# Kernel tuning notes

Hardware: AMD Instinct MI355X
Metric: run time of the kernel (lower is better)

Reference implementation:

```python
import jax, jax.numpy as jnp
import numpy as np

D_MODEL = 1024
D_INTERNAL = 1024
B, T = 4, 2048
ROPE_BASE = 10000.0


def _rotate_half(x):
    h = x.shape[-1] // 2
    return jnp.concatenate([-x[..., h:], x[..., :h]], axis=-1)


def _justnorm(x):
    return x / jnp.linalg.norm(x, axis=-1, keepdims=True)


def setup_inputs() -> dict:
    key = jax.random.key(0)
    k1, k2 = jax.random.split(key)
    stdev = 1.0 / (D_MODEL + D_INTERNAL) ** 0.5
    qkv_w = jax.random.uniform(k1, (3 * D_INTERNAL, D_MODEL), minval=-stdev, maxval=stdev, dtype=jnp.float32)
    qkv_w = _justnorm(qkv_w)  # source normalizes qkv rows at init
    sqk = (D_MODEL ** -0.5) * jnp.ones((D_INTERNAL,), dtype=jnp.float32)  # sqk_init_scaling * ones
    input_vecs = jax.random.normal(k2, (B, T, D_MODEL), dtype=jnp.float32)
    return {"input_vecs": input_vecs, "qkv_w": qkv_w, "sqk": sqk}


def reference(input_vecs, qkv_w, sqk):
    d_model = input_vecs.shape[-1]
    d_int = qkv_w.shape[0] // 3
    t_len = input_vecs.shape[-2]

    # QKV projection: F.linear(x, W) == x @ W.T
    qkv = jnp.einsum('btc,dc->btd', input_vecs, qkv_w)
    Q, K, V = jnp.split(qkv, 3, axis=-1)  # each [B, T, d_int]

    # Rotary embeddings over full d_int
    inv_freq = 1.0 / (ROPE_BASE ** (jnp.arange(0, d_int, 2, dtype=jnp.float32) / d_int))
    t = jnp.arange(t_len, dtype=jnp.float32)
    freqs = t[:, None] * inv_freq[None, :]              # [T, d_int/2]
    emb = jnp.concatenate([freqs, freqs], axis=-1)      # [T, d_int]
    cos, sin = jnp.cos(emb), jnp.sin(emb)
    Q = Q * cos + _rotate_half(Q) * sin
    K = K * cos + _rotate_half(K) * sin

    # L2 QK-norm with learned per-channel scale (sqk * (1.0 / sqk_init_scaling))
    sqk_eff = sqk * (d_model ** 0.5)
    Q = _justnorm(Q) * sqk_eff
    K = _justnorm(K) * sqk_eff

    # SDPA, eval path: causal, dropout=0, scale = C ** 0.5
    scale = d_model ** 0.5
    scores = jnp.einsum('bqd,bkd->bqk', Q, K) * scale   # [B, T, T]
    causal = jnp.tril(jnp.ones((t_len, t_len), dtype=bool))
    scores = jnp.where(causal[None, :, :], scores, -jnp.inf)
    attn = jax.nn.softmax(scores, axis=-1)
    out = jnp.einsum('bqk,bkd->bqd', attn, V)
    return out
```

## Files before the change

### kernel.cpp

```cpp
#include <hip/hip_runtime.h>

typedef unsigned short u16;
typedef short s16x8 __attribute__((ext_vector_type(8)));
typedef float f32x4 __attribute__((ext_vector_type(4)));

__device__ __forceinline__ u16 f2bf(float f) {
    union { float f; unsigned u; } v; v.f = f;
    unsigned r = v.u + 0x7FFFu + ((v.u >> 16) & 1u);
    return (u16)(r >> 16);
}
__device__ __forceinline__ float bf2f(u16 h) {
    union { unsigned u; float f; } v; v.u = ((unsigned)h) << 16;
    return v.f;
}
__device__ __forceinline__ u16 f2h(float f) {
    _Float16 h = (_Float16)f;
    union { _Float16 h; u16 u; } v; v.h = h; return v.u;
}
__device__ __forceinline__ float h2f(u16 u) {
    union { u16 u; _Float16 h; } v; v.u = u; return (float)v.h;
}

__device__ __forceinline__ void gl_lds16(const u16* g, u16* l) {
    __builtin_amdgcn_global_load_lds(
        (const __attribute__((address_space(1))) void*)g,
        (__attribute__((address_space(3))) void*)l,
        16, 0, 0);
}

__device__ __forceinline__ s16x8 ldfrag(const u16* base, int row, int kk, int fq) {
    int cb = ((kk << 6) + (fq << 4)) ^ ((row & 7) << 4);
    return *reinterpret_cast<const s16x8*>(base + row * 64 + (cb >> 1));
}

#define MFMA16(a, b, c) __builtin_amdgcn_mfma_f32_16x16x32_bf16((a), (b), (c), 0, 0, 0)

__global__ __launch_bounds__(256)
void prep(const float* __restrict__ x, const float* __restrict__ w,
          u16* __restrict__ xb, u16* __restrict__ wb, u16* __restrict__ trig) {
    const int bid = blockIdx.x;
    if (bid < 2048) {
        int i = (bid * 256 + threadIdx.x) * 4;
        const int stride = 2048 * 256 * 4;
        for (; i < 8192 * 1024; i += stride) {
            float4 v = *reinterpret_cast<const float4*>(x + i);
            ushort4 o;
            o.x = f2bf(v.x); o.y = f2bf(v.y); o.z = f2bf(v.z); o.w = f2bf(v.w);
            *reinterpret_cast<ushort4*>(xb + i) = o;
        }
    } else if (bid < 2816) {
        int i = ((bid - 2048) * 256 + threadIdx.x) * 4;
        const int stride = 768 * 256 * 4;
        for (; i < 3072 * 1024; i += stride) {
            float4 v = *reinterpret_cast<const float4*>(w + i);
            ushort4 o;
            o.x = f2bf(v.x); o.y = f2bf(v.y); o.z = f2bf(v.z); o.w = f2bf(v.w);
            *reinterpret_cast<ushort4*>(wb + i) = o;
        }
    } else {
        const int t = bid - 2816;
        const float L = 0.025952563241307517f;
        u16* row = trig + (size_t)t * 1024;
#pragma unroll
        for (int i = 0; i < 2; ++i) {
            int d = threadIdx.x + i * 256;
            float invf = exp2f(-(float)d * L);
            float ang = (float)t * invf;
            float s, c;
            sincosf(ang, &s, &c);
            row[d] = f2h(c);
            row[512 + d] = f2h(s);
        }
    }
}

template <int MODE, typename CT>
__global__ __launch_bounds__(256, 2)
void gemm_bt(const u16* __restrict__ A, const u16* __restrict__ B, CT* __restrict__ C,
             u16* __restrict__ VT, float* __restrict__ psum,
             int K, int lda, int ldb, int ldc, long sA, long sB, long sC) {
    int bx, by, bz;
    if (MODE == 0) {
        int bid = blockIdx.x;
        int xcd = bid & 7, idx = bid >> 3;
        int r = idx >> 6, w2 = idx & 63;
        bx = r * 8 + (w2 & 7);
        by = xcd * 8 + (w2 >> 3);
        bz = 0;
    } else if (MODE == 1) {
        int bid = blockIdx.x;
        int xcd = bid & 7;
        bz = xcd >> 1;
        int j = (xcd & 1) * 68 + (bid >> 3);
        by = (int)((sqrtf(8.f * j + 1.f) - 1.f) * 0.5f);
        while ((by + 1) * (by + 2) / 2 <= j) ++by;
        while (by * (by + 1) / 2 > j) --by;
        bx = j - by * (by + 1) / 2;
    } else {
        int bid = blockIdx.x;
        int xcd = bid & 7;
        bz = xcd >> 1;
        int j = (xcd & 1) * 64 + (bid >> 3);
        by = 15 - (j >> 3);
        bx = j & 7;
    }
    A += (size_t)bz * sA; B += (size_t)bz * sB; C += (size_t)bz * sC;
    int kend = K;
    if (MODE == 2) { int kl = (by + 1) * 128; kend = kl < K ? kl : K; }
    const int NT = kend >> 6;

    __shared__ u16 lds[32768];

    const int tid  = threadIdx.x;
    const int lane = tid & 63;
    const int wave = tid >> 6;
    const int wr = (wave >> 1) * 64;
    const int wc = (wave & 1) * 64;
    const int fr = lane & 15;
    const int fq = lane >> 4;
    const int tm = by * 128, tn = bx * 128;

    const int srow = tid >> 3;
    const int gco  = (((tid & 7) ^ (srow & 7)) << 3);
    const u16* aR[4]; const u16* bR[4];
#pragma unroll
    for (int j = 0; j < 4; ++j) {
        aR[j] = A + (size_t)(tm + j * 32 + srow) * lda + gco;
        bR[j] = B + (size_t)(tn + j * 32 + srow) * ldb + gco;
    }

#define STAGE(b2, k0) do {                                                        \
    _Pragma("unroll") for (int j = 0; j < 4; ++j)                                 \
        gl_lds16(aR[j] + (k0), lds + (b2) * 16384 + j * 2048 + tid * 8);          \
    _Pragma("unroll") for (int j = 0; j < 4; ++j)                                 \
        gl_lds16(bR[j] + (k0), lds + (b2) * 16384 + 8192 + j * 2048 + tid * 8);   \
  } while (0)

    f32x4 acc[4][4];
#pragma unroll
    for (int m = 0; m < 4; ++m)
#pragma unroll
        for (int n = 0; n < 4; ++n) acc[m][n] = {0.f, 0.f, 0.f, 0.f};

    STAGE(0, 0);
    if (NT > 1) STAGE(1, 64);

    for (int t = 0; t < NT; ++t) {
        const int buf = t & 1;
        if (t + 1 < NT) { asm volatile("s_waitcnt vmcnt(8)" ::: "memory"); }
        else            { asm volatile("s_waitcnt vmcnt(0)" ::: "memory"); }
        __builtin_amdgcn_s_barrier();
        __builtin_amdgcn_sched_barrier(0);

        const u16* Ab = lds + buf * 16384;
        const u16* Bb = Ab + 8192;
        s16x8 bf0[4], bf1[4];
#pragma unroll
        for (int n = 0; n < 4; ++n) {
            bf0[n] = ldfrag(Bb, wc + n * 16 + fr, 0, fq);
            bf1[n] = ldfrag(Bb, wc + n * 16 + fr, 1, fq);
        }
        __builtin_amdgcn_s_setprio(1);
#pragma unroll
        for (int m = 0; m < 4; ++m) {
            s16x8 a0 = ldfrag(Ab, wr + m * 16 + fr, 0, fq);
            s16x8 a1 = ldfrag(Ab, wr + m * 16 + fr, 1, fq);
#pragma unroll
            for (int n = 0; n < 4; ++n) {
                acc[m][n] = MFMA16(a0, bf0[n], acc[m][n]);
                acc[m][n] = MFMA16(a1, bf1[n], acc[m][n]);
            }
        }
        __builtin_amdgcn_s_setprio(0);
        __builtin_amdgcn_sched_barrier(0);
        __builtin_amdgcn_s_barrier();
        if (t + 2 < NT) STAGE(buf, (t + 2) << 6);
    }
#undef STAGE

    if (MODE == 0 && tn >= 2048) {
#pragma unroll
        for (int m = 0; m < 4; ++m)
#pragma unroll
            for (int n = 0; n < 4; ++n)
#pragma unroll
                for (int r = 0; r < 4; ++r) {
                    int row = tm + wr + m * 16 + fq * 4 + r;
                    int col = tn + wc + n * 16 + fr;
                    VT[((size_t)(row >> 11)) * 2097152 + (size_t)(col - 2048) * 2048 + (row & 2047)]
                        = f2bf(acc[m][n][r]);
                }
    } else if (MODE == 1) {
        u16* P = (u16*)C;
#pragma unroll
        for (int m = 0; m < 4; ++m) {
#pragma unroll
            for (int r = 0; r < 4; ++r) {
                int row = tm + wr + m * 16 + fq * 4 + r;
                float rs = 0.f;
#pragma unroll
                for (int n = 0; n < 4; ++n) {
                    int col = tn + wc + n * 16 + fr;
                    float p = (col <= row) ? __expf(32.f * acc[m][n][r] - 32.f) : 0.f;
                    u16 pb = f2bf(p);
                    P[(size_t)row * 2048 + col] = pb;
                    rs += bf2f(pb);
                }
                rs += __shfl_xor(rs, 1);
                rs += __shfl_xor(rs, 2);
                rs += __shfl_xor(rs, 4);
                rs += __shfl_xor(rs, 8);
                if (fr == 0)
                    psum[((size_t)bz * 32 + bx * 2 + (wave & 1)) * 2048 + row] = rs;
            }
        }
    } else if (MODE == 2) {
        float* rinv = (float*)lds;
        if (tid < 128) {
            int row = tm + tid;
            int ns = 2 * (by + 1);
            float s = 0.f;
            for (int j = 0; j < ns; ++j)
                s += psum[((size_t)bz * 32 + j) * 2048 + row];
            rinv[tid] = 1.f / s;
        }
        __syncthreads();
#pragma unroll
        for (int m = 0; m < 4; ++m) {
#pragma unroll
            for (int r = 0; r < 4; ++r) {
                int lrow = wr + m * 16 + fq * 4 + r;
                float inv = rinv[lrow];
                int row = tm + lrow;
#pragma unroll
                for (int n = 0; n < 4; ++n) {
                    int col = tn + wc + n * 16 + fr;
                    C[(size_t)row * ldc + col] = acc[m][n][r] * inv;
                }
            }
        }
    } else {
#pragma unroll
        for (int m = 0; m < 4; ++m)
#pragma unroll
            for (int n = 0; n < 4; ++n)
#pragma unroll
                for (int r = 0; r < 4; ++r) {
                    int row = tm + wr + m * 16 + fq * 4 + r;
                    int col = tn + wc + n * 16 + fr;
                    C[(size_t)row * ldc + col] = (CT)f2bf(acc[m][n][r]);
                }
    }
}

__global__ __launch_bounds__(256)
void rope_norm(u16* __restrict__ qk, const float* __restrict__ sqk,
               const u16* __restrict__ trig) {
    const int row = blockIdx.x;
    const int t = row & 2047;
    u16* qp = qk + (size_t)row * 2048;
    u16* kp = qp + 1024;
    const u16* tb = trig + (size_t)t * 1024;
    const int d = threadIdx.x << 1;

    union U2 { uint u; u16 h[2]; };
    U2 qc0, qc1, kc0, kc1, cc, ss;
    qc0.u = *reinterpret_cast<const uint*>(qp + d);
    qc1.u = *reinterpret_cast<const uint*>(qp + 512 + d);
    kc0.u = *reinterpret_cast<const uint*>(kp + d);
    kc1.u = *reinterpret_cast<const uint*>(kp + 512 + d);
    cc.u  = *reinterpret_cast<const uint*>(tb + d);
    ss.u  = *reinterpret_cast<const uint*>(tb + 512 + d);

    float nq0[2], nq1[2], nk0[2], nk1[2];
    float ssq_q = 0.f, ssq_k = 0.f;
#pragma unroll
    for (int j = 0; j < 2; ++j) {
        float c = h2f(cc.h[j]), s = h2f(ss.h[j]);
        float q0 = bf2f(qc0.h[j]), q1 = bf2f(qc1.h[j]);
        float k0 = bf2f(kc0.h[j]), k1 = bf2f(kc1.h[j]);
        nq0[j] = q0 * c - q1 * s;
        nq1[j] = q1 * c + q0 * s;
        nk0[j] = k0 * c - k1 * s;
        nk1[j] = k1 * c + k0 * s;
        ssq_q += nq0[j] * nq0[j] + nq1[j] * nq1[j];
        ssq_k += nk0[j] * nk0[j] + nk1[j] * nk1[j];
    }

#pragma unroll
    for (int off = 32; off; off >>= 1) {
        ssq_q += __shfl_xor(ssq_q, off);
        ssq_k += __shfl_xor(ssq_k, off);
    }
    __shared__ float red[8];
    int wave = threadIdx.x >> 6, lane = threadIdx.x & 63;
    if (lane == 0) { red[wave] = ssq_q; red[4 + wave] = ssq_k; }
    __syncthreads();
    float rq = rsqrtf(red[0] + red[1] + red[2] + red[3]);
    float rk = rsqrtf(red[4] + red[5] + red[6] + red[7]);

    float2 sq0 = *reinterpret_cast<const float2*>(sqk + d);
    float2 sq1 = *reinterpret_cast<const float2*>(sqk + 512 + d);
    float s0[2] = {sq0.x * 32.f, sq0.y * 32.f};
    float s1[2] = {sq1.x * 32.f, sq1.y * 32.f};

    U2 oq0, oq1, ok0, ok1;
#pragma unroll
    for (int j = 0; j < 2; ++j) {
        oq0.h[j] = f2bf(nq0[j] * rq * s0[j]);
        oq1.h[j] = f2bf(nq1[j] * rq * s1[j]);
        ok0.h[j] = f2bf(nk0[j] * rk * s0[j]);
        ok1.h[j] = f2bf(nk1[j] * rk * s1[j]);
    }
    *reinterpret_cast<uint*>(qp + d)       = oq0.u;
    *reinterpret_cast<uint*>(qp + 512 + d) = oq1.u;
    *reinterpret_cast<uint*>(kp + d)       = ok0.u;
    *reinterpret_cast<uint*>(kp + 512 + d) = ok1.u;
}

extern "C" void kernel_launch(void* const* d_in, const int* in_sizes, int n_in,
                              void* d_out, int out_size, void* d_ws, size_t ws_size,
                              hipStream_t stream) {
    const float* x   = (const float*)d_in[0];
    const float* w   = (const float*)d_in[1];
    const float* sqk = (const float*)d_in[2];
    float* out = (float*)d_out;

    const size_t SZ_XB  = (size_t)8192 * 1024 * 2;
    const size_t SZ_WB  = (size_t)3072 * 1024 * 2;
    const size_t SZ_QK  = (size_t)8192 * 2048 * 2;
    const size_t SZ_VT  = (size_t)4 * 1024 * 2048 * 2;
    const size_t SZ_P   = (size_t)4 * 2048 * 2048 * 2;
    const size_t SZ_TR  = (size_t)2048 * 1024 * 2;
    const size_t SZ_PS  = (size_t)4 * 32 * 2048 * 4;
    if (ws_size < SZ_XB + SZ_WB + SZ_QK + SZ_VT + SZ_P + SZ_TR + SZ_PS) return;

    char* ws = (char*)d_ws;
    u16*   xb   = (u16*)ws;   ws += SZ_XB;
    u16*   wb   = (u16*)ws;   ws += SZ_WB;
    u16*   qk   = (u16*)ws;   ws += SZ_QK;
    u16*   VT   = (u16*)ws;   ws += SZ_VT;
    u16*   P    = (u16*)ws;   ws += SZ_P;
    u16*   trig = (u16*)ws;   ws += SZ_TR;
    float* psum = (float*)ws;

    prep<<<4864, 256, 0, stream>>>(x, w, xb, wb, trig);

    gemm_bt<0, u16><<<dim3(1536, 1, 1), 256, 0, stream>>>(
        xb, wb, qk, VT, nullptr, 1024, 1024, 1024, 2048, 0, 0, 0);

    rope_norm<<<8192, 256, 0, stream>>>(qk, sqk, trig);

    gemm_bt<1, u16><<<dim3(544, 1, 1), 256, 0, stream>>>(
        qk, qk + 1024, P, nullptr, psum, 1024, 2048, 2048, 2048,
        (long)2048 * 2048, (long)2048 * 2048, (long)2048 * 2048);

    gemm_bt<2, float><<<dim3(512, 1, 1), 256, 0, stream>>>(
        P, VT, out, nullptr, psum, 2048, 2048, 2048, 1024,
        (long)2048 * 2048, (long)1024 * 2048, (long)2048 * 1024);
}
```

Measured before the change: 146.1 us.

## Fuse RoPE and QK-norm into QKV GEMM epilogue via permuted weight rows

The Q/K weight rows are permuted during bf16 conversion so that each RoPE pair lands in the same thread's accumulator tile. The QKV GEMM epilogue can then apply rotation and the sqk scale, and emit partial sums of squares. A small reduce kernel turns those sums into per-row inverse norms, which the QK^T GEMM epilogue applies to its scores. This removes the separate rope_norm pass that re-read and re-wrote Q/K, at the cost of strided scalar trig loads in the epilogue and an extra tiny launch. Q/K are now stored unnormalized in bf16, which may slightly change rounding.

```diff
diff --git a/kernel.cpp b/kernel.cpp
--- a/kernel.cpp
+++ b/kernel.cpp
@@ -49,13 +49,22 @@
             *reinterpret_cast<ushort4*>(xb + i) = o;
         }
     } else if (bid < 2816) {
-        int i = ((bid - 2048) * 256 + threadIdx.x) * 4;
-        const int stride = 768 * 256 * 4;
-        for (; i < 3072 * 1024; i += stride) {
-            float4 v = *reinterpret_cast<const float4*>(w + i);
+        const int rbase = (bid - 2048) * 4;
+#pragma unroll
+        for (int rr = 0; rr < 4; ++rr) {
+            int row = rbase + rr;
+            int src;
+            if (row < 2048) {
+                int sec = row >> 10, rp = row & 1023;
+                int j = ((rp >> 5) << 4) | (rp & 15);
+                src = (sec << 10) + ((((rp >> 4) & 1) == 0) ? j : j + 512);
+            } else {
+                src = row;
+            }
+            float4 v = *reinterpret_cast<const float4*>(w + (size_t)src * 1024 + threadIdx.x * 4);
             ushort4 o;
             o.x = f2bf(v.x); o.y = f2bf(v.y); o.z = f2bf(v.z); o.w = f2bf(v.w);
-            *reinterpret_cast<ushort4*>(wb + i) = o;
+            *reinterpret_cast<ushort4*>(wb + (size_t)row * 1024 + threadIdx.x * 4) = o;
         }
     } else {
         const int t = bid - 2816;
@@ -74,10 +83,23 @@
     }
 }
 
+__global__ __launch_bounds__(256)
+void norm_reduce(const float* __restrict__ ssqbuf, float* __restrict__ rqk) {
+    const int row = blockIdx.x * 256 + threadIdx.x;
+    float sq = 0.f, sk = 0.f;
+#pragma unroll
+    for (int s = 0; s < 16; ++s) sq += ssqbuf[(size_t)s * 8192 + row];
+#pragma unroll
+    for (int s = 16; s < 32; ++s) sk += ssqbuf[(size_t)s * 8192 + row];
+    rqk[row] = rsqrtf(sq);
+    rqk[8192 + row] = rsqrtf(sk);
+}
+
 template <int MODE, typename CT>
 __global__ __launch_bounds__(256, 2)
 void gemm_bt(const u16* __restrict__ A, const u16* __restrict__ B, CT* __restrict__ C,
-             u16* __restrict__ VT, float* __restrict__ psum,
+             u16* __restrict__ VT, float* __restrict__ psum, const float* __restrict__ rqk,
+             const u16* __restrict__ trig, const float* __restrict__ sqk,
              int K, int lda, int ldb, int ldc, long sA, long sB, long sC) {
     int bx, by, bz;
     if (MODE == 0) {
@@ -190,18 +212,60 @@
                     VT[((size_t)(row >> 11)) * 2097152 + (size_t)(col - 2048) * 2048 + (row & 2047)]
                         = f2bf(acc[m][n][r]);
                 }
+    } else if (MODE == 0) {
+        int c0a = tn + wc + fr;
+        int c0b = c0a + 32;
+        int csa = c0a & 1023, csb = c0b & 1023;
+        int ja = ((csa >> 5) << 4) | (csa & 15);
+        int jb = ((csb >> 5) << 4) | (csb & 15);
+        float ea0 = sqk[ja] * 32.f,       ea1 = sqk[ja + 512] * 32.f;
+        float eb0 = sqk[jb] * 32.f,       eb1 = sqk[jb + 512] * 32.f;
+#pragma unroll
+        for (int m = 0; m < 4; ++m) {
+#pragma unroll
+            for (int r = 0; r < 4; ++r) {
+                int row = tm + wr + m * 16 + fq * 4 + r;
+                const u16* tb = trig + (size_t)(row & 2047) * 1024;
+                float ca = h2f(tb[ja]), sa = h2f(tb[512 + ja]);
+                float cb = h2f(tb[jb]), sb = h2f(tb[512 + jb]);
+                float v0 = acc[m][0][r], v1 = acc[m][1][r];
+                float v2 = acc[m][2][r], v3 = acc[m][3][r];
+                float r0 = v0 * ca - v1 * sa;
+                float r1 = v1 * ca + v0 * sa;
+                float r2 = v2 * cb - v3 * sb;
+                float r3 = v3 * cb + v2 * sb;
+                float ss = r0 * r0 + r1 * r1 + r2 * r2 + r3 * r3;
+                ss += __shfl_xor(ss, 1);
+                ss += __shfl_xor(ss, 2);
+                ss += __shfl_xor(ss, 4);
+                ss += __shfl_xor(ss, 8);
+                u16* qrow = (u16*)C + (size_t)row * 2048;
+                qrow[c0a]      = f2bf(r0 * ea0);
+                qrow[c0a + 16] = f2bf(r1 * ea1);
+                qrow[c0b]      = f2bf(r2 * eb0);
+                qrow[c0b + 16] = f2bf(r3 * eb1);
+                if (fr == 0)
+                    psum[(size_t)(bx * 2 + (wave & 1)) * 8192 + row] = ss;
+            }
+        }
     } else if (MODE == 1) {
         u16* P = (u16*)C;
+        float rkc[4];
+#pragma unroll
+        for (int n = 0; n < 4; ++n)
+            rkc[n] = rqk[8192 + bz * 2048 + tn + wc + n * 16 + fr];
 #pragma unroll
         for (int m = 0; m < 4; ++m) {
 #pragma unroll
             for (int r = 0; r < 4; ++r) {
                 int row = tm + wr + m * 16 + fq * 4 + r;
+                float rqr = rqk[bz * 2048 + row];
                 float rs = 0.f;
 #pragma unroll
                 for (int n = 0; n < 4; ++n) {
                     int col = tn + wc + n * 16 + fr;
-                    float p = (col <= row) ? __expf(32.f * acc[m][n][r] - 32.f) : 0.f;
+                    float u = acc[m][n][r] * rqr * rkc[n];
+                    float p = (col <= row) ? __expf(32.f * u - 32.f) : 0.f;
                     u16 pb = f2bf(p);
                     P[(size_t)row * 2048 + col] = pb;
                     rs += bf2f(pb);
@@ -239,83 +303,7 @@
                 }
             }
         }
-    } else {
-#pragma unroll
-        for (int m = 0; m < 4; ++m)
-#pragma unroll
-            for (int n = 0; n < 4; ++n)
-#pragma unroll
-                for (int r = 0; r < 4; ++r) {
-                    int row = tm + wr + m * 16 + fq * 4 + r;
-                    int col = tn + wc + n * 16 + fr;
-                    C[(size_t)row * ldc + col] = (CT)f2bf(acc[m][n][r]);
-                }
-    }
-}
-
-__global__ __launch_bounds__(256)
-void rope_norm(u16* __restrict__ qk, const float* __restrict__ sqk,
-               const u16* __restrict__ trig) {
-    const int row = blockIdx.x;
-    const int t = row & 2047;
-    u16* qp = qk + (size_t)row * 2048;
-    u16* kp = qp + 1024;
-    const u16* tb = trig + (size_t)t * 1024;
-    const int d = threadIdx.x << 1;
-
-    union U2 { uint u; u16 h[2]; };
-    U2 qc0, qc1, kc0, kc1, cc, ss;
-    qc0.u = *reinterpret_cast<const uint*>(qp + d);
-    qc1.u = *reinterpret_cast<const uint*>(qp + 512 + d);
-    kc0.u = *reinterpret_cast<const uint*>(kp + d);
-    kc1.u = *reinterpret_cast<const uint*>(kp + 512 + d);
-    cc.u  = *reinterpret_cast<const uint*>(tb + d);
-    ss.u  = *reinterpret_cast<const uint*>(tb + 512 + d);
-
-    float nq0[2], nq1[2], nk0[2], nk1[2];
-    float ssq_q = 0.f, ssq_k = 0.f;
-#pragma unroll
-    for (int j = 0; j < 2; ++j) {
-        float c = h2f(cc.h[j]), s = h2f(ss.h[j]);
-        float q0 = bf2f(qc0.h[j]), q1 = bf2f(qc1.h[j]);
-        float k0 = bf2f(kc0.h[j]), k1 = bf2f(kc1.h[j]);
-        nq0[j] = q0 * c - q1 * s;
-        nq1[j] = q1 * c + q0 * s;
-        nk0[j] = k0 * c - k1 * s;
-        nk1[j] = k1 * c + k0 * s;
-        ssq_q += nq0[j] * nq0[j] + nq1[j] * nq1[j];
-        ssq_k += nk0[j] * nk0[j] + nk1[j] * nk1[j];
-    }
-
-#pragma unroll
-    for (int off = 32; off; off >>= 1) {
-        ssq_q += __shfl_xor(ssq_q, off);
-        ssq_k += __shfl_xor(ssq_k, off);
-    }
-    __shared__ float red[8];
-    int wave = threadIdx.x >> 6, lane = threadIdx.x & 63;
-    if (lane == 0) { red[wave] = ssq_q; red[4 + wave] = ssq_k; }
-    __syncthreads();
-    float rq = rsqrtf(red[0] + red[1] + red[2] + red[3]);
-    float rk = rsqrtf(red[4] + red[5] + red[6] + red[7]);
-
-    float2 sq0 = *reinterpret_cast<const float2*>(sqk + d);
-    float2 sq1 = *reinterpret_cast<const float2*>(sqk + 512 + d);
-    float s0[2] = {sq0.x * 32.f, sq0.y * 32.f};
-    float s1[2] = {sq1.x * 32.f, sq1.y * 32.f};
-
-    U2 oq0, oq1, ok0, ok1;
-#pragma unroll
-    for (int j = 0; j < 2; ++j) {
-        oq0.h[j] = f2bf(nq0[j] * rq * s0[j]);
-        oq1.h[j] = f2bf(nq1[j] * rq * s1[j]);
-        ok0.h[j] = f2bf(nk0[j] * rk * s0[j]);
-        ok1.h[j] = f2bf(nk1[j] * rk * s1[j]);
-    }
-    *reinterpret_cast<uint*>(qp + d)       = oq0.u;
-    *reinterpret_cast<uint*>(qp + 512 + d) = oq1.u;
-    *reinterpret_cast<uint*>(kp + d)       = ok0.u;
-    *reinterpret_cast<uint*>(kp + 512 + d) = ok1.u;
+    }
 }
 
 extern "C" void kernel_launch(void* const* d_in, const int* in_sizes, int n_in,
@@ -333,29 +321,36 @@
     const size_t SZ_P   = (size_t)4 * 2048 * 2048 * 2;
     const size_t SZ_TR  = (size_t)2048 * 1024 * 2;
     const size_t SZ_PS  = (size_t)4 * 32 * 2048 * 4;
-    if (ws_size < SZ_XB + SZ_WB + SZ_QK + SZ_VT + SZ_P + SZ_TR + SZ_PS) return;
+    const size_t SZ_SSQ = (size_t)32 * 8192 * 4;
+    const size_t SZ_RQK = (size_t)2 * 8192 * 4;
+    if (ws_size < SZ_XB + SZ_WB + SZ_QK + SZ_VT + SZ_P + SZ_TR + SZ_PS + SZ_SSQ + SZ_RQK) return;
 
     char* ws = (char*)d_ws;
-    u16*   xb   = (u16*)ws;   ws += SZ_XB;
-    u16*   wb   = (u16*)ws;   ws += SZ_WB;
-    u16*   qk   = (u16*)ws;   ws += SZ_QK;
-    u16*   VT   = (u16*)ws;   ws += SZ_VT;
-    u16*   P    = (u16*)ws;   ws += SZ_P;
-    u16*   trig = (u16*)ws;   ws += SZ_TR;
-    float* psum = (float*)ws;
+    u16*   xb     = (u16*)ws;   ws += SZ_XB;
+    u16*   wb     = (u16*)ws;   ws += SZ_WB;
+    u16*   qk     = (u16*)ws;   ws += SZ_QK;
+    u16*   VT     = (u16*)ws;   ws += SZ_VT;
+    u16*   P      = (u16*)ws;   ws += SZ_P;
+    u16*   trig   = (u16*)ws;   ws += SZ_TR;
+    float* psum   = (float*)ws; ws += SZ_PS;
+    float* ssqbuf = (float*)ws; ws += SZ_SSQ;
+    float* rqk    = (float*)ws;
 
     prep<<<4864, 256, 0, stream>>>(x, w, xb, wb, trig);
 
     gemm_bt<0, u16><<<dim3(1536, 1, 1), 256, 0, stream>>>(
-        xb, wb, qk, VT, nullptr, 1024, 1024, 1024, 2048, 0, 0, 0);
-
-    rope_norm<<<8192, 256, 0, stream>>>(qk, sqk, trig);
+        xb, wb, qk, VT, ssqbuf, nullptr, trig, sqk,
+        1024, 1024, 1024, 2048, 0, 0, 0);
+
+    norm_reduce<<<dim3(32, 1, 1), 256, 0, stream>>>(ssqbuf, rqk);
 
     gemm_bt<1, u16><<<dim3(544, 1, 1), 256, 0, stream>>>(
-        qk, qk + 1024, P, nullptr, psum, 1024, 2048, 2048, 2048,
+        qk, qk + 1024, P, nullptr, psum, rqk, nullptr, nullptr,
+        1024, 2048, 2048, 2048,
         (long)2048 * 2048, (long)2048 * 2048, (long)2048 * 2048);
 
     gemm_bt<2, float><<<dim3(512, 1, 1), 256, 0, stream>>>(
-        P, VT, out, nullptr, psum, 2048, 2048, 2048, 1024,
+        P, VT, out, nullptr, psum, nullptr, nullptr, nullptr,
+        2048, 2048, 2048, 1024,
         (long)2048 * 2048, (long)1024 * 2048, (long)2048 * 1024);
 }
```

After: 154.2 us. +5.6%, slower.
